# Kernel optimization log

Hardware: AMD Instinct MI355X
Metric: run time of the kernel (lower is better)

## Reference

```python
import jax, jax.numpy as jnp
import numpy as np

NUM_ITERS = 2      # num_iters default
NEG_SLOPE = 0.2    # LeakyReLU slope in GAT attention
NEG_INF = -1e9

N, E, B, H, K, L = 204800, 6144000, 4096, 8, 30, 50


def setup_inputs() -> dict:
    key = jax.random.key(0)
    ks = jax.random.split(key, 14)
    return {
        "target_features": jax.random.normal(ks[0], (N, 8), jnp.float32),
        "feature_dist_graph": jax.random.normal(ks[1], (E, 8), jnp.float32),
        "rij_dist_pairs": jax.random.uniform(ks[2], (E,), jnp.float32),
        "b_scope": jax.random.randint(ks[3], (N, K), 0, E + 1, jnp.int32),
        "start_end_env": jax.random.randint(ks[4], (N, K), 0, N + 1, jnp.int32),
        "l_scope": jax.random.randint(ks[5], (B, L), 0, N + 1, jnp.int32),
        "edge_src": jax.random.randint(ks[6], (E,), 0, N + 1, jnp.int32),
        "W_emb": jax.random.normal(ks[7], (8, H), jnp.float32),
        "b_emb": jax.random.normal(ks[8], (H,), jnp.float32),
        "W_dist": jax.random.normal(ks[9], (9, H), jnp.float32),
        "b_dist": jax.random.normal(ks[10], (H,), jnp.float32),
        "W_gat": jax.random.normal(ks[11], (H, H), jnp.float32),
        "a_src": jax.random.normal(ks[12], (H,), jnp.float32),
        "a_dst": jax.random.normal(ks[13], (H,), jnp.float32),
    }


def reference(target_features, feature_dist_graph, rij_dist_pairs,
              b_scope, start_end_env, l_scope, edge_src,
              W_emb, b_emb, W_dist, b_dist, W_gat, a_src, a_dst):
    # node embedding: [N, 8] -> [N, H]
    h = target_features @ W_emb + b_emb
    # edge (feature+distance) embedding: [E, 9] -> [E, H]
    msg = jnp.concatenate([feature_dist_graph, rij_dist_pairs[:, None]], axis=1) @ W_dist + b_dist
    zero = jnp.zeros((1, h.shape[1]), h.dtype)
    h = jnp.concatenate([zero, h], axis=0)          # zero row for 1-based / padded indices
    pad_mask = b_scope > 0                           # padded neighbor slots point at row 0
    for _ in range(NUM_ITERS):
        nbr_self = h[start_end_env]                  # getConnectedFeatures: [N, K, H] (target repeated)
        msg0 = jnp.concatenate([zero, msg], axis=0)  # zero row for padded edge indices
        nbr_msg = msg0[b_scope]                      # gathered neighbor messages [N, K, H]
        # GAT attention over the K neighbor slots
        z_s = nbr_self @ W_gat                       # [N, K, H]
        z_m = nbr_msg @ W_gat                        # [N, K, H]
        e = jax.nn.leaky_relu(z_s @ a_src + z_m @ a_dst, NEG_SLOPE)  # [N, K]
        e = jnp.where(pad_mask, e, NEG_INF)
        alpha = jax.nn.softmax(e, axis=1)            # [N, K]
        out = jnp.einsum('nk,nkh->nh', alpha, z_m)   # attention-weighted aggregate [N, H]
        h = jnp.concatenate([zero, jax.nn.elu(out)], axis=0)  # [N+1, H]
        # updateConnectedDict: scatter node states back to per-edge messages
        msg = h[edge_src]                            # [E, H]
    # readout: gather per-graph feature rows and sum -> mol_vecs [B, H]
    return h[l_scope].sum(axis=1)
```

## Files before the change

### kernel.cpp

```cpp
#include <hip/hip_runtime.h>

typedef float f32x4 __attribute__((ext_vector_type(4)));

#define NEG_SLOPE 0.2f
#define NEG_INF   -1e9f

__global__ void prep_embed(const float* __restrict__ fdg,
                           const float* __restrict__ rij,
                           const float* __restrict__ W_dist,
                           const float* __restrict__ b_dist,
                           const float* __restrict__ W_gat,
                           const float* __restrict__ a_src,
                           const float* __restrict__ tf,
                           const float* __restrict__ W_emb,
                           const float* __restrict__ b_emb,
                           float* __restrict__ rec,
                           float* __restrict__ h_a,
                           float* __restrict__ h_b,
                           float* __restrict__ t0,
                           float* __restrict__ t1,
                           int E, int N, int nb_edge) {
    __shared__ float sW[72];
    __shared__ float sb[8];
    __shared__ float sWg[64];
    __shared__ float s_vec[8];
    int tid = threadIdx.x;
    bool edge_block = (blockIdx.x < nb_edge);
    if (edge_block) {
        if (tid < 72) sW[tid] = W_dist[tid];
        else if (tid < 80) sb[tid - 72] = b_dist[tid - 72];
    } else {
        if (tid < 64) sW[tid] = W_emb[tid];
        else if (tid < 72) sb[tid - 64] = b_emb[tid - 64];
        if (tid >= 128 && tid < 192) sWg[tid - 128] = W_gat[tid - 128];
    }
    __syncthreads();
    if (!edge_block && tid < 8) {
        float s = 0.f;
        #pragma unroll
        for (int j = 0; j < 8; ++j) s += sWg[tid * 8 + j] * a_src[j];
        s_vec[tid] = s;
    }
    __syncthreads();

    if (edge_block) {
        int e = blockIdx.x * blockDim.x + tid;
        if (e >= E) return;
        const f32x4* fr = reinterpret_cast<const f32x4*>(fdg + (size_t)e * 8);
        f32x4 g0 = fr[0], g1 = fr[1];
        float rv = rij[e];
        float msg[8];
        #pragma unroll
        for (int j = 0; j < 8; ++j) {
            float s = sb[j];
            #pragma unroll
            for (int i = 0; i < 4; ++i) s += g0[i] * sW[i * 8 + j];
            #pragma unroll
            for (int i = 0; i < 4; ++i) s += g1[i] * sW[(4 + i) * 8 + j];
            s += rv * sW[64 + j];
            msg[j] = s;
        }
        f32x4* op = reinterpret_cast<f32x4*>(rec + (size_t)e * 8);
        f32x4 m0 = {msg[0], msg[1], msg[2], msg[3]};
        f32x4 m1 = {msg[4], msg[5], msg[6], msg[7]};
        op[0] = m0; op[1] = m1;
    } else {
        int n = (blockIdx.x - nb_edge) * blockDim.x + tid;
        if (n >= N) return;
        if (n == 0) {
            #pragma unroll
            for (int j = 0; j < 8; ++j) { h_a[j] = 0.f; h_b[j] = 0.f; }
            t0[0] = 0.f;
            t1[0] = 0.f;
        }
        const f32x4* tfr = reinterpret_cast<const f32x4*>(tf + (size_t)n * 8);
        f32x4 a = tfr[0], b = tfr[1];
        float x[8] = {a[0], a[1], a[2], a[3], b[0], b[1], b[2], b[3]};
        float out[8];
        #pragma unroll
        for (int j = 0; j < 8; ++j) out[j] = sb[j];
        #pragma unroll
        for (int i = 0; i < 8; ++i)
            #pragma unroll
            for (int j = 0; j < 8; ++j)
                out[j] += x[i] * sW[i * 8 + j];
        float t = 0.f;
        #pragma unroll
        for (int p = 0; p < 8; ++p) t += out[p] * s_vec[p];
        t0[n + 1] = t;
        f32x4* hr = reinterpret_cast<f32x4*>(h_a + (size_t)(n + 1) * 8);
        f32x4 o0 = {out[0], out[1], out[2], out[3]};
        f32x4 o1 = {out[4], out[5], out[6], out[7]};
        hr[0] = o0;
        hr[1] = o1;
    }
}

__device__ __forceinline__ void finish_node(const float msg[8], float t_se, float em,
                                            bool has, bool vk, int lane, int node,
                                            const float* __restrict__ sWg,
                                            const float* __restrict__ s_as,
                                            float* __restrict__ h_next,
                                            float* __restrict__ t_next) {
    float ee = t_se + em;
    ee = (ee >= 0.f) ? ee : NEG_SLOPE * ee;
    float e = has ? ee : (vk ? NEG_INF : -3e38f);

    float m = e;
    #pragma unroll
    for (int off = 16; off; off >>= 1) m = fmaxf(m, __shfl_xor(m, off, 32));
    float p = vk ? expf(e - m) : 0.f;
    float denom = p;
    #pragma unroll
    for (int off = 16; off; off >>= 1) denom += __shfl_xor(denom, off, 32);
    float alpha = p / denom;

    float agg[8];
    #pragma unroll
    for (int j = 0; j < 8; ++j) agg[j] = alpha * msg[j];
    #pragma unroll
    for (int off = 16; off; off >>= 1)
        #pragma unroll
        for (int j = 0; j < 8; ++j) agg[j] += __shfl_xor(agg[j], off, 32);

    if (lane < 8) {
        float o = 0.f;
        #pragma unroll
        for (int i = 0; i < 8; ++i) o += agg[i] * sWg[i * 8 + lane];
        o = (o > 0.f) ? o : (expf(o) - 1.f);
        h_next[(size_t)(node + 1) * 8 + lane] = o;
        if (t_next) {
            float tv = o * s_as[lane];
            tv += __shfl_xor(tv, 1, 32);
            tv += __shfl_xor(tv, 2, 32);
            tv += __shfl_xor(tv, 4, 32);
            if (lane == 0) t_next[node + 1] = tv;
        }
    }
}

__global__ void gat_iter1_rec(const float* __restrict__ t0,
                              float* __restrict__ h1,
                              float* __restrict__ t1,
                              const int* __restrict__ b_scope,
                              const int* __restrict__ se_env,
                              const float* __restrict__ rec,
                              const float* __restrict__ W_gat,
                              const float* __restrict__ a_src,
                              const float* __restrict__ a_dst,
                              int N, int K) {
    __shared__ float sWg[64];
    __shared__ float s_as[8];
    __shared__ float s_ad[8];
    int tid = threadIdx.x;
    if (tid < 64) sWg[tid] = W_gat[tid];
    __syncthreads();
    if (tid < 8) {
        float s = 0.f;
        #pragma unroll
        for (int j = 0; j < 8; ++j) s += sWg[tid * 8 + j] * a_src[j];
        s_as[tid] = s;
    } else if (tid < 16) {
        int i = tid - 8;
        float s = 0.f;
        #pragma unroll
        for (int j = 0; j < 8; ++j) s += sWg[i * 8 + j] * a_dst[j];
        s_ad[i] = s;
    }
    __syncthreads();

    int node = blockIdx.x * 8 + (tid >> 5);
    int lane = tid & 31;
    if (node >= N) return;
    bool vk = (lane < K);

    int bs = 0, se = 0;
    if (vk) {
        bs = b_scope[(size_t)node * K + lane];
        se = se_env[(size_t)node * K + lane];
    }
    bool has = vk && (bs > 0);
    float t_se = vk ? t0[se] : 0.f;

    f32x4 m0 = {0,0,0,0}, m1 = {0,0,0,0};
    if (has) {
        const f32x4* rp = reinterpret_cast<const f32x4*>(rec + (size_t)(bs - 1) * 8);
        m0 = rp[0]; m1 = rp[1];
    }
    float msg[8] = {m0[0], m0[1], m0[2], m0[3], m1[0], m1[1], m1[2], m1[3]};
    float em = 0.f;
    #pragma unroll
    for (int j = 0; j < 8; ++j) em += msg[j] * s_ad[j];

    finish_node(msg, t_se, em, has, vk, lane, node, sWg, s_as, h1, t1);
}

__global__ void gat_iter1_fb(const float* __restrict__ t0,
                             float* __restrict__ h1,
                             float* __restrict__ t1,
                             const int* __restrict__ b_scope,
                             const int* __restrict__ se_env,
                             const float* __restrict__ fdg,
                             const float* __restrict__ rij,
                             const float* __restrict__ W_dist,
                             const float* __restrict__ b_dist,
                             const float* __restrict__ W_gat,
                             const float* __restrict__ a_src,
                             const float* __restrict__ a_dst,
                             int N, int K) {
    __shared__ float sWg[64];
    __shared__ float s_as[8];
    __shared__ float s_ad[8];
    __shared__ float sWd[72];
    __shared__ float sbd[8];
    int tid = threadIdx.x;
    if (tid < 64) sWg[tid] = W_gat[tid];
    if (tid >= 64 && tid < 136) sWd[tid - 64] = W_dist[tid - 64];
    if (tid >= 136 && tid < 144) sbd[tid - 136] = b_dist[tid - 136];
    __syncthreads();
    if (tid < 8) {
        float s = 0.f;
        #pragma unroll
        for (int j = 0; j < 8; ++j) s += sWg[tid * 8 + j] * a_src[j];
        s_as[tid] = s;
    } else if (tid < 16) {
        int i = tid - 8;
        float s = 0.f;
        #pragma unroll
        for (int j = 0; j < 8; ++j) s += sWg[i * 8 + j] * a_dst[j];
        s_ad[i] = s;
    }
    __syncthreads();

    int node = blockIdx.x * 8 + (tid >> 5);
    int lane = tid & 31;
    if (node >= N) return;
    bool vk = (lane < K);

    int bs = 0, se = 0;
    if (vk) {
        bs = b_scope[(size_t)node * K + lane];
        se = se_env[(size_t)node * K + lane];
    }
    bool has = vk && (bs > 0);
    float t_se = vk ? t0[se] : 0.f;

    float msg[8];
    #pragma unroll
    for (int j = 0; j < 8; ++j) msg[j] = 0.f;
    float em = 0.f;
    if (has) {
        const f32x4* fr = reinterpret_cast<const f32x4*>(fdg + (size_t)(bs - 1) * 8);
        f32x4 g0 = fr[0], g1 = fr[1];
        float rv = rij[bs - 1];
        #pragma unroll
        for (int j = 0; j < 8; ++j) {
            float s = sbd[j];
            #pragma unroll
            for (int i = 0; i < 4; ++i) s += g0[i] * sWd[i * 8 + j];
            #pragma unroll
            for (int i = 0; i < 4; ++i) s += g1[i] * sWd[(4 + i) * 8 + j];
            s += rv * sWd[64 + j];
            msg[j] = s;
        }
        #pragma unroll
        for (int j = 0; j < 8; ++j) em += msg[j] * s_ad[j];
    }
    finish_node(msg, t_se, em, has, vk, lane, node, sWg, s_as, h1, t1);
}

__global__ void gat_iter2(const float* __restrict__ h1,
                          const float* __restrict__ t1,
                          float* __restrict__ h2,
                          const int* __restrict__ b_scope,
                          const int* __restrict__ se_env,
                          const int* __restrict__ edge_src,
                          const float* __restrict__ W_gat,
                          const float* __restrict__ a_dst,
                          int N, int K) {
    __shared__ float sWg[64];
    __shared__ float s_ad[8];
    int tid = threadIdx.x;
    if (tid < 64) sWg[tid] = W_gat[tid];
    __syncthreads();
    if (tid < 8) {
        float s = 0.f;
        #pragma unroll
        for (int j = 0; j < 8; ++j) s += sWg[tid * 8 + j] * a_dst[j];
        s_ad[tid] = s;
    }
    __syncthreads();

    int lane = tid & 31;
    int g = blockIdx.x * 8 + (tid >> 5);
    int nA = g * 2, nB = g * 2 + 1;
    if (nA >= N) return;
    bool hasBn = (nB < N);
    bool vk = (lane < K);

    int bsA = 0, seA = 0, bsB = 0, seB = 0;
    if (vk) {
        bsA = b_scope[(size_t)nA * K + lane];
        seA = se_env[(size_t)nA * K + lane];
        if (hasBn) {
            bsB = b_scope[(size_t)nB * K + lane];
            seB = se_env[(size_t)nB * K + lane];
        }
    }
    bool hasA = vk && (bsA > 0);
    bool hasB = vk && hasBn && (bsB > 0);

    float tA = vk ? t1[seA] : 0.f;
    float tB = (vk && hasBn) ? t1[seB] : 0.f;

    int srcA = 0, srcB = 0;
    if (hasA) srcA = edge_src[bsA - 1];
    if (hasB) srcB = edge_src[bsB - 1];

    f32x4 a0 = {0,0,0,0}, a1 = {0,0,0,0}, b0 = {0,0,0,0}, b1 = {0,0,0,0};
    if (hasA) {
        const f32x4* mr = reinterpret_cast<const f32x4*>(h1 + (size_t)srcA * 8);
        a0 = mr[0]; a1 = mr[1];
    }
    if (hasB) {
        const f32x4* mr = reinterpret_cast<const f32x4*>(h1 + (size_t)srcB * 8);
        b0 = mr[0]; b1 = mr[1];
    }

    float msgA[8] = {a0[0], a0[1], a0[2], a0[3], a1[0], a1[1], a1[2], a1[3]};
    float emA = 0.f;
    #pragma unroll
    for (int j = 0; j < 8; ++j) emA += msgA[j] * s_ad[j];
    finish_node(msgA, tA, emA, hasA, vk, lane, nA, sWg, nullptr, h2, nullptr);
    if (hasBn) {
        float msgB[8] = {b0[0], b0[1], b0[2], b0[3], b1[0], b1[1], b1[2], b1[3]};
        float emB = 0.f;
        #pragma unroll
        for (int j = 0; j < 8; ++j) emB += msgB[j] * s_ad[j];
        finish_node(msgB, tB, emB, hasB, vk, lane, nB, sWg, nullptr, h2, nullptr);
    }
}

__global__ void readout_kernel(const float* __restrict__ h,
                               const int* __restrict__ l_scope,
                               float* __restrict__ out, int B, int L) {
    int gid = blockIdx.x * blockDim.x + threadIdx.x;
    int b = gid >> 3;
    int j = gid & 7;
    if (b >= B) return;
    float s = 0.f;
    for (int l = 0; l < L; ++l) {
        int idx = l_scope[(size_t)b * L + l];
        s += h[(size_t)idx * 8 + j];
    }
    out[(size_t)b * 8 + j] = s;
}

extern "C" void kernel_launch(void* const* d_in, const int* in_sizes, int n_in,
                              void* d_out, int out_size, void* d_ws, size_t ws_size,
                              hipStream_t stream) {
    const float* tf      = (const float*)d_in[0];
    const float* fdg     = (const float*)d_in[1];
    const float* rij     = (const float*)d_in[2];
    const int* b_scope   = (const int*)d_in[3];
    const int* start_env = (const int*)d_in[4];
    const int* l_scope   = (const int*)d_in[5];
    const int* edge_src  = (const int*)d_in[6];
    const float* W_emb   = (const float*)d_in[7];
    const float* b_emb   = (const float*)d_in[8];
    const float* W_dist  = (const float*)d_in[9];
    const float* b_dist  = (const float*)d_in[10];
    const float* W_gat   = (const float*)d_in[11];
    const float* a_src   = (const float*)d_in[12];
    const float* a_dst   = (const float*)d_in[13];
    float* out = (float*)d_out;

    const int N = in_sizes[0] / 8;
    const int E = in_sizes[1] / 8;
    const int K = in_sizes[3] / N;
    const int L = 50;
    const int B = in_sizes[5] / L;

    size_t rec_f = (size_t)E * 8;
    size_t need  = (rec_f + 2 * (size_t)(N + 1) * 8 + 2 * (size_t)(N + 1)) * 4;
    bool use_rec = (ws_size >= need);

    float* base = (float*)d_ws;
    float* rec  = base;
    size_t off  = use_rec ? rec_f : 0;
    float* h_a  = base + off;  off += (size_t)(N + 1) * 8;
    float* h_b  = base + off;  off += (size_t)(N + 1) * 8;
    float* t0v  = base + off;  off += (size_t)(N + 1);
    float* t1v  = base + off;

    const int nb_edge = (E + 255) / 256;
    const int nb_node = (N + 255) / 256;

    if (use_rec) {
        prep_embed<<<nb_edge + nb_node, 256, 0, stream>>>(
            fdg, rij, W_dist, b_dist, W_gat, a_src,
            tf, W_emb, b_emb, rec, h_a, h_b, t0v, t1v, E, N, nb_edge);
        gat_iter1_rec<<<(N + 7) / 8, 256, 0, stream>>>(t0v, h_b, t1v,
                                                       b_scope, start_env, rec,
                                                       W_gat, a_src, a_dst, N, K);
    } else {
        prep_embed<<<nb_node, 256, 0, stream>>>(
            fdg, rij, W_dist, b_dist, W_gat, a_src,
            tf, W_emb, b_emb, rec, h_a, h_b, t0v, t1v, 0, N, 0);
        gat_iter1_fb<<<(N + 7) / 8, 256, 0, stream>>>(t0v, h_b, t1v,
                                                      b_scope, start_env,
                                                      fdg, rij,
                                                      W_dist, b_dist, W_gat,
                                                      a_src, a_dst, N, K);
    }

    const int g2_blocks = ((N + 1) / 2 + 7) / 8;
    gat_iter2<<<g2_blocks, 256, 0, stream>>>(h_b, t1v, h_a, b_scope, start_env,
                                             edge_src, W_gat, a_dst, N, K);

    readout_kernel<<<(B * 8 + 255) / 256, 256, 0, stream>>>(h_a, l_scope, out, B, L);
}
```

Baseline: 432.1 us.

## Precompute composed edge_src[b_scope] indices in prep kernel, interleaved with edge embedding

Adds a third block type to the prep kernel that resolves each neighbor slot's b_scope entry through edge_src into a precomputed source-node index array. Slot blocks are interleaved with the edge-embedding blocks so this random gather can overlap with the streaming work. gat_iter2 then reads this array directly, which removes one dependent random load from its critical path. In exchange it needs extra workspace and adds an N*K int write and read.

```diff
diff --git a/kernel.cpp b/kernel.cpp
--- a/kernel.cpp
+++ b/kernel.cpp
@@ -7,6 +7,8 @@
 
 __global__ void prep_embed(const float* __restrict__ fdg,
                            const float* __restrict__ rij,
+                           const int* __restrict__ b_scope,
+                           const int* __restrict__ edge_src,
                            const float* __restrict__ W_dist,
                            const float* __restrict__ b_dist,
                            const float* __restrict__ W_gat,
@@ -15,27 +17,44 @@
                            const float* __restrict__ W_emb,
                            const float* __restrict__ b_emb,
                            float* __restrict__ rec,
+                           int* __restrict__ src_idx,
                            float* __restrict__ h_a,
                            float* __restrict__ h_b,
                            float* __restrict__ t0,
                            float* __restrict__ t1,
-                           int E, int N, int nb_edge) {
+                           int E, int NK, int N,
+                           int nb_pair, int nb_edge, int nb_slot) {
     __shared__ float sW[72];
     __shared__ float sb[8];
     __shared__ float sWg[64];
     __shared__ float s_vec[8];
     int tid = threadIdx.x;
-    bool edge_block = (blockIdx.x < nb_edge);
-    if (edge_block) {
+    int bid = blockIdx.x;
+
+    int type, widx;
+    if (bid < 2 * nb_pair) {
+        type = bid & 1;
+        widx = bid >> 1;
+    } else {
+        int r = bid - 2 * nb_pair;
+        if (r < nb_edge - nb_pair)      { type = 0; widx = nb_pair + r; }
+        else {
+            r -= (nb_edge - nb_pair);
+            if (r < nb_slot - nb_pair)  { type = 1; widx = nb_pair + r; }
+            else                        { type = 2; widx = r - (nb_slot - nb_pair); }
+        }
+    }
+
+    if (type == 0) {
         if (tid < 72) sW[tid] = W_dist[tid];
         else if (tid < 80) sb[tid - 72] = b_dist[tid - 72];
-    } else {
+    } else if (type == 2) {
         if (tid < 64) sW[tid] = W_emb[tid];
         else if (tid < 72) sb[tid - 64] = b_emb[tid - 64];
         if (tid >= 128 && tid < 192) sWg[tid - 128] = W_gat[tid - 128];
     }
     __syncthreads();
-    if (!edge_block && tid < 8) {
+    if (type == 2 && tid < 8) {
         float s = 0.f;
         #pragma unroll
         for (int j = 0; j < 8; ++j) s += sWg[tid * 8 + j] * a_src[j];
@@ -43,8 +62,8 @@
     }
     __syncthreads();
 
-    if (edge_block) {
-        int e = blockIdx.x * blockDim.x + tid;
+    if (type == 0) {
+        int e = widx * 256 + tid;
         if (e >= E) return;
         const f32x4* fr = reinterpret_cast<const f32x4*>(fdg + (size_t)e * 8);
         f32x4 g0 = fr[0], g1 = fr[1];
@@ -64,8 +83,13 @@
         f32x4 m0 = {msg[0], msg[1], msg[2], msg[3]};
         f32x4 m1 = {msg[4], msg[5], msg[6], msg[7]};
         op[0] = m0; op[1] = m1;
+    } else if (type == 1) {
+        int s = widx * 256 + tid;
+        if (s >= NK) return;
+        int bs = b_scope[s];
+        src_idx[s] = (bs > 0) ? edge_src[bs - 1] : -1;
     } else {
-        int n = (blockIdx.x - nb_edge) * blockDim.x + tid;
+        int n = widx * 256 + tid;
         if (n >= N) return;
         if (n == 0) {
             #pragma unroll
@@ -269,9 +293,11 @@
     finish_node(msg, t_se, em, has, vk, lane, node, sWg, s_as, h1, t1);
 }
 
+template <bool SRCIDX>
 __global__ void gat_iter2(const float* __restrict__ h1,
                           const float* __restrict__ t1,
                           float* __restrict__ h2,
+                          const int* __restrict__ src_idx,
                           const int* __restrict__ b_scope,
                           const int* __restrict__ se_env,
                           const int* __restrict__ edge_src,
@@ -298,24 +324,34 @@
     bool hasBn = (nB < N);
     bool vk = (lane < K);
 
-    int bsA = 0, seA = 0, bsB = 0, seB = 0;
-    if (vk) {
-        bsA = b_scope[(size_t)nA * K + lane];
-        seA = se_env[(size_t)nA * K + lane];
-        if (hasBn) {
-            bsB = b_scope[(size_t)nB * K + lane];
-            seB = se_env[(size_t)nB * K + lane];
-        }
-    }
-    bool hasA = vk && (bsA > 0);
-    bool hasB = vk && hasBn && (bsB > 0);
+    int srcA = -1, srcB = -1, seA = 0, seB = 0;
+    if (SRCIDX) {
+        if (vk) {
+            srcA = src_idx[(size_t)nA * K + lane];
+            seA  = se_env[(size_t)nA * K + lane];
+            if (hasBn) {
+                srcB = src_idx[(size_t)nB * K + lane];
+                seB  = se_env[(size_t)nB * K + lane];
+            }
+        }
+    } else {
+        int bsA = 0, bsB = 0;
+        if (vk) {
+            bsA = b_scope[(size_t)nA * K + lane];
+            seA = se_env[(size_t)nA * K + lane];
+            if (hasBn) {
+                bsB = b_scope[(size_t)nB * K + lane];
+                seB = se_env[(size_t)nB * K + lane];
+            }
+        }
+        if (vk && bsA > 0) srcA = edge_src[bsA - 1];
+        if (vk && hasBn && bsB > 0) srcB = edge_src[bsB - 1];
+    }
+    bool hasA = vk && (srcA >= 0);
+    bool hasB = vk && hasBn && (srcB >= 0);
 
     float tA = vk ? t1[seA] : 0.f;
     float tB = (vk && hasBn) ? t1[seB] : 0.f;
-
-    int srcA = 0, srcB = 0;
-    if (hasA) srcA = edge_src[bsA - 1];
-    if (hasB) srcB = edge_src[bsB - 1];
 
     f32x4 a0 = {0,0,0,0}, a1 = {0,0,0,0}, b0 = {0,0,0,0}, b1 = {0,0,0,0};
     if (hasA) {
@@ -380,9 +416,11 @@
     const int K = in_sizes[3] / N;
     const int L = 50;
     const int B = in_sizes[5] / L;
+    const int NK = N * K;
 
     size_t rec_f = (size_t)E * 8;
-    size_t need  = (rec_f + 2 * (size_t)(N + 1) * 8 + 2 * (size_t)(N + 1)) * 4;
+    size_t need  = (rec_f + (size_t)NK
+                    + 2 * (size_t)(N + 1) * 8 + 2 * (size_t)(N + 1)) * 4;
     bool use_rec = (ws_size >= need);
 
     float* base = (float*)d_ws;
@@ -391,32 +429,42 @@
     float* h_a  = base + off;  off += (size_t)(N + 1) * 8;
     float* h_b  = base + off;  off += (size_t)(N + 1) * 8;
     float* t0v  = base + off;  off += (size_t)(N + 1);
-    float* t1v  = base + off;
+    float* t1v  = base + off;  off += (size_t)(N + 1);
+    int* src_idx = (int*)(base + off);
 
     const int nb_edge = (E + 255) / 256;
+    const int nb_slot = (NK + 255) / 256;
     const int nb_node = (N + 255) / 256;
+    const int nb_pair = (nb_edge < nb_slot) ? nb_edge : nb_slot;
 
     if (use_rec) {
-        prep_embed<<<nb_edge + nb_node, 256, 0, stream>>>(
-            fdg, rij, W_dist, b_dist, W_gat, a_src,
-            tf, W_emb, b_emb, rec, h_a, h_b, t0v, t1v, E, N, nb_edge);
+        const int grid = nb_edge + nb_slot + nb_node;
+        prep_embed<<<grid, 256, 0, stream>>>(
+            fdg, rij, b_scope, edge_src, W_dist, b_dist, W_gat, a_src,
+            tf, W_emb, b_emb, rec, src_idx, h_a, h_b, t0v, t1v,
+            E, NK, N, nb_pair, nb_edge, nb_slot);
         gat_iter1_rec<<<(N + 7) / 8, 256, 0, stream>>>(t0v, h_b, t1v,
                                                        b_scope, start_env, rec,
                                                        W_gat, a_src, a_dst, N, K);
+        const int g2_blocks = ((N + 1) / 2 + 7) / 8;
+        gat_iter2<true><<<g2_blocks, 256, 0, stream>>>(h_b, t1v, h_a,
+                                                       src_idx, b_scope, start_env,
+                                                       edge_src, W_gat, a_dst, N, K);
     } else {
         prep_embed<<<nb_node, 256, 0, stream>>>(
-            fdg, rij, W_dist, b_dist, W_gat, a_src,
-            tf, W_emb, b_emb, rec, h_a, h_b, t0v, t1v, 0, N, 0);
+            fdg, rij, b_scope, edge_src, W_dist, b_dist, W_gat, a_src,
+            tf, W_emb, b_emb, rec, (int*)rec, h_a, h_b, t0v, t1v,
+            0, 0, N, 0, 0, 0);
         gat_iter1_fb<<<(N + 7) / 8, 256, 0, stream>>>(t0v, h_b, t1v,
                                                       b_scope, start_env,
                                                       fdg, rij,
                                                       W_dist, b_dist, W_gat,
                                                       a_src, a_dst, N, K);
-    }
-
-    const int g2_blocks = ((N + 1) / 2 + 7) / 8;
-    gat_iter2<<<g2_blocks, 256, 0, stream>>>(h_b, t1v, h_a, b_scope, start_env,
-                                             edge_src, W_gat, a_dst, N, K);
+        const int g2_blocks = ((N + 1) / 2 + 7) / 8;
+        gat_iter2<false><<<g2_blocks, 256, 0, stream>>>(h_b, t1v, h_a,
+                                                        (const int*)rec, b_scope, start_env,
+                                                        edge_src, W_gat, a_dst, N, K);
+    }
 
     readout_kernel<<<(B * 8 + 255) / 256, 256, 0, stream>>>(h_a, l_scope, out, B, L);
 }
```

Measured after the change: 406.8 us, median of 2. -5.9%, faster.
